# Kernel optimization log

Measured on AMD Instinct MI355X. Metric: run time of the kernel, lower is better.

## Reference

```python
import jax, jax.numpy as jnp
import numpy as np


def setup_inputs() -> dict:
    key = jax.random.key(0)
    ks = jax.random.split(key, 7)
    B, P, D = 4, 2048, 1024
    s = 1.0 / np.sqrt(D)
    return {
        "x":  jax.random.normal(ks[0], (B, P, D), dtype=jnp.float32),
        "Wq": jax.random.normal(ks[1], (D, D), dtype=jnp.float32) * s,
        "bq": jnp.zeros((D,), dtype=jnp.float32),
        "Wk": jax.random.normal(ks[2], (D, D), dtype=jnp.float32) * s,
        "bk": jnp.zeros((D,), dtype=jnp.float32),
        "Wv": jax.random.normal(ks[3], (D, D), dtype=jnp.float32) * s,
        "bv": jnp.zeros((D,), dtype=jnp.float32),
    }


def reference(x, Wq, bq, Wk, bk, Wv, bv):
    # x: [B, P, D]; Linear uses W stored torch-style [out, in]: y = x @ W.T + b
    b, p, d = x.shape
    q = jnp.einsum("bpd,ed->bpe", x, Wq) + bq
    k = jnp.einsum("bpd,ed->bpe", x, Wk) + bk
    v = jnp.einsum("bpd,ed->bpe", x, Wv) + bv
    attn = jnp.einsum("bqd,bkd->bqk", q, k)  # [B, P, P]
    causal = jnp.triu(jnp.ones((p, p), dtype=bool), k=1)  # True above diagonal
    attn = jnp.where(causal, -jnp.inf, attn)
    attn = attn / jnp.sqrt(jnp.asarray(d, dtype=attn.dtype))
    scores = jax.nn.softmax(attn, axis=-1)
    # dropout is identity in eval/deterministic mode
    return jnp.einsum("bqk,bkd->bqd", scores, v)
```

## Files before the change

kernel.cpp:

```cpp
#include <hip/hip_runtime.h>
#include <hip/hip_bf16.h>


typedef __attribute__((ext_vector_type(8))) short bf16x8;
typedef __attribute__((ext_vector_type(4))) float f32x4;

__device__ __forceinline__ unsigned short f2bf(float f) {
    union { float f; unsigned u; } v; v.f = f;
    unsigned r = v.u + 0x7FFF + ((v.u >> 16) & 1);
    return (unsigned short)(r >> 16);
}

__device__ __forceinline__ void gload_lds16(const unsigned short* g, unsigned short* l) {
    __builtin_amdgcn_global_load_lds(
        (const __attribute__((address_space(1))) unsigned int*)g,
        (__attribute__((address_space(3))) unsigned int*)l, 16, 0, 0);
}

__global__ void convert_kernel(const float* __restrict__ x,  const float* __restrict__ wq,
                               const float* __restrict__ wk, const float* __restrict__ wv,
                               const float* __restrict__ bq, const float* __restrict__ bk,
                               const float* __restrict__ bv,
                               unsigned short* __restrict__ xb, unsigned short* __restrict__ wqkvb,
                               float* __restrict__ bqkv, float* __restrict__ lsum) {
    long t = (long)blockIdx.x * blockDim.x + threadIdx.x;
    long idx = t * 4;
    const float* src; unsigned short* dst; long off;
    if      (idx <  8388608) { src = x;  dst = xb;            off = idx;            }
    else if (idx <  9437184) { src = wq; dst = wqkvb;         off = idx -  8388608; }
    else if (idx < 10485760) { src = wk; dst = wqkvb+1048576; off = idx -  9437184; }
    else if (idx < 11534336) { src = wv; dst = wqkvb+2097152; off = idx - 10485760; }
    else return;
    float4 v = *(const float4*)(src + off);
    ushort4 o = make_ushort4(f2bf(v.x), f2bf(v.y), f2bf(v.z), f2bf(v.w));
    *(ushort4*)(dst + off) = o;
    if (t < 768) {
        long o2 = t * 4;
        float4 b;
        if      (o2 < 1024) b = *(const float4*)(bq + o2);
        else if (o2 < 2048) b = *(const float4*)(bk + o2 - 1024);
        else                b = *(const float4*)(bv + o2 - 2048);
        *(float4*)(bqkv + o2) = b;
    }
    if (t >= 1024 && t < 3072) {
        float4 z = make_float4(0.f, 0.f, 0.f, 0.f);
        *(float4*)(lsum + (t - 1024) * 4) = z;
    }
}

__device__ __forceinline__ void stage(const unsigned short* gA, long lda,
                                      const unsigned short* gB, long ldb,
                                      unsigned short* As, unsigned short* Bs,
                                      int w, int k0) {
#pragma unroll
    for (int s = 0; s < 4; ++s) {
        gload_lds16(gA + k0 + (long)(s * 8) * lda, &As[(w * 32 + s * 8) * 64]);
        gload_lds16(gB + k0 + (long)(s * 8) * ldb, &Bs[(w * 32 + s * 8) * 64]);
    }
}

template<bool SWAP>
__device__ __forceinline__ void mfma_tile(const unsigned short* As, const unsigned short* Bs,
                                          int wr, int wc, int ln, int pr0, int pr1,
                                          f32x4 (&acc)[4][4]) {
#pragma unroll
    for (int kk = 0; kk < 2; ++kk) {
        const int pr = kk ? pr1 : pr0;
        bf16x8 af[4], bfr[4];
#pragma unroll
        for (int i = 0; i < 4; ++i)
            af[i] = *(const bf16x8*)(&As[(wr + i * 16 + ln) * 64 + pr]);
#pragma unroll
        for (int j = 0; j < 4; ++j)
            bfr[j] = *(const bf16x8*)(&Bs[(wc + j * 16 + ln) * 64 + pr]);
#pragma unroll
        for (int i = 0; i < 4; ++i)
#pragma unroll
            for (int j = 0; j < 4; ++j)
                acc[i][j] = SWAP
                    ? __builtin_amdgcn_mfma_f32_16x16x32_bf16(bfr[j], af[i], acc[i][j], 0, 0, 0)
                    : __builtin_amdgcn_mfma_f32_16x16x32_bf16(af[i], bfr[j], acc[i][j], 0, 0, 0);
    }
}

template<bool SWAP>
__device__ __forceinline__ void kloop_db(const unsigned short* gA, long lda,
                                         const unsigned short* gB, long ldb,
                                         unsigned short* As0, unsigned short* Bs0,
                                         unsigned short* As1, unsigned short* Bs1,
                                         int w, int lane, int Keff, f32x4 (&acc)[4][4]) {
    const int q  = lane >> 4;
    const int ln = lane & 15;
    const int wr = (w >> 1) * 64;
    const int wc = (w & 1) * 64;
    const int pr0 = ((q)     ^ (ln & 7)) * 8;
    const int pr1 = ((q + 4) ^ (ln & 7)) * 8;
    stage(gA, lda, gB, ldb, As0, Bs0, w, 0);
    __syncthreads();
    for (int k0 = 0; k0 < Keff; k0 += 128) {
        stage(gA, lda, gB, ldb, As1, Bs1, w, k0 + 64);
        mfma_tile<SWAP>(As0, Bs0, wr, wc, ln, pr0, pr1, acc);
        __syncthreads();
        if (k0 + 128 < Keff)
            stage(gA, lda, gB, ldb, As0, Bs0, w, k0 + 128);
        mfma_tile<SWAP>(As1, Bs1, wr, wc, ln, pr0, pr1, acc);
        __syncthreads();
    }
}

__global__ __launch_bounds__(256, 2)
void gemm_qkv(const unsigned short* __restrict__ X,
              const unsigned short* __restrict__ W,
              unsigned short* __restrict__ QK,
              unsigned short* __restrict__ VT,
              const float* __restrict__ bias) {
    const int n0 = blockIdx.x * 128;
    const int m0 = blockIdx.y * 128;
    __shared__ __align__(16) unsigned short As0[128 * 64], Bs0[128 * 64];
    __shared__ __align__(16) unsigned short As1[128 * 64], Bs1[128 * 64];
    const int tid = threadIdx.x, lane = tid & 63, w = tid >> 6;
    const int q = lane >> 4, ln = lane & 15;
    const int wr = (w >> 1) * 64, wc = (w & 1) * 64;
    const int srow = lane >> 3, sc = (lane & 7) ^ srow;
    const unsigned short* gA = X + (long)(m0 + w * 32 + srow) * 1024 + sc * 8;
    const unsigned short* gB = W + (long)(n0 + w * 32 + srow) * 1024 + sc * 8;
    f32x4 acc[4][4] = {};
    if (n0 >= 2048) {
        kloop_db<false>(gA, 1024, gB, 1024, As0, Bs0, As1, Bs1, w, lane, 1024, acc);
#pragma unroll
        for (int j = 0; j < 4; ++j) {
            const int e = n0 - 2048 + wc + j * 16 + ln;
            const float bc = bias[n0 + wc + j * 16 + ln];
#pragma unroll
            for (int i = 0; i < 4; ++i) {
                const int m = m0 + wr + i * 16 + q * 4;
                ushort4 o = make_ushort4(f2bf(acc[i][j][0] + bc), f2bf(acc[i][j][1] + bc),
                                         f2bf(acc[i][j][2] + bc), f2bf(acc[i][j][3] + bc));
                *(ushort4*)(VT + (long)e * 8192 + m) = o;
            }
        }
    } else {
        kloop_db<true>(gA, 1024, gB, 1024, As0, Bs0, As1, Bs1, w, lane, 1024, acc);
#pragma unroll
        for (int j = 0; j < 4; ++j) {
            const float4 bc = *(const float4*)(bias + n0 + wc + j * 16 + q * 4);
#pragma unroll
            for (int i = 0; i < 4; ++i) {
                const int m = m0 + wr + i * 16 + ln;
                const int n = n0 + wc + j * 16 + q * 4;
                ushort4 o = make_ushort4(f2bf(acc[i][j][0] + bc.x), f2bf(acc[i][j][1] + bc.y),
                                         f2bf(acc[i][j][2] + bc.z), f2bf(acc[i][j][3] + bc.w));
                *(ushort4*)(QK + (long)m * 2048 + n) = o;
            }
        }
    }
}

__global__ __launch_bounds__(256, 2)
void gemm_scores(const unsigned short* __restrict__ QK,
                 unsigned short* __restrict__ P,
                 float* __restrict__ lsum) {
    const int t = blockIdx.x;
    int i = (int)((sqrtf(8.0f * t + 1.0f) - 1.0f) * 0.5f);
    while ((i + 1) * (i + 2) / 2 <= t) ++i;
    while (i * (i + 1) / 2 > t) --i;
    const int j = t - i * (i + 1) / 2;
    const int m0 = i * 128, n0 = j * 128, z = blockIdx.y;
    const unsigned short* Qz = QK + (long)z * 2048 * 2048;
    const unsigned short* Kz = Qz + 1024;
    unsigned short* Pz = P + (long)z * 2048 * 2048;
    float* lz = lsum + z * 2048;

    __shared__ __align__(16) unsigned short As0[128 * 64], Bs0[128 * 64];
    __shared__ __align__(16) unsigned short As1[128 * 64], Bs1[128 * 64];
    const int tid = threadIdx.x, lane = tid & 63, w = tid >> 6;
    const int q = lane >> 4, ln = lane & 15;
    const int wr = (w >> 1) * 64, wc = (w & 1) * 64;
    const int srow = lane >> 3, sc = (lane & 7) ^ srow;
    const unsigned short* gA = Qz + (long)(m0 + w * 32 + srow) * 2048 + sc * 8;
    const unsigned short* gB = Kz + (long)(n0 + w * 32 + srow) * 2048 + sc * 8;
    f32x4 acc[4][4] = {};
    kloop_db<true>(gA, 2048, gB, 2048, As0, Bs0, As1, Bs1, w, lane, 1024, acc);

    const float scale = 0.03125f;
#pragma unroll
    for (int i2 = 0; i2 < 4; ++i2) {
        const int m = m0 + wr + i2 * 16 + ln;
        float rs = 0.f;
#pragma unroll
        for (int j2 = 0; j2 < 4; ++j2) {
            const int n = n0 + wc + j2 * 16 + q * 4;
            float p0 = (n     <= m) ? __expf(acc[i2][j2][0] * scale) : 0.f;
            float p1 = (n + 1 <= m) ? __expf(acc[i2][j2][1] * scale) : 0.f;
            float p2 = (n + 2 <= m) ? __expf(acc[i2][j2][2] * scale) : 0.f;
            float p3 = (n + 3 <= m) ? __expf(acc[i2][j2][3] * scale) : 0.f;
            rs += (p0 + p1) + (p2 + p3);
            ushort4 o = make_ushort4(f2bf(p0), f2bf(p1), f2bf(p2), f2bf(p3));
            *(ushort4*)(Pz + (long)m * 2048 + n) = o;
        }
        rs += __shfl_xor(rs, 16); rs += __shfl_xor(rs, 32);
        if (lane < 16) atomicAdd(&lz[m], rs);
    }
}

__global__ __launch_bounds__(256, 2)
void gemm_pv(const unsigned short* __restrict__ P,
             const unsigned short* __restrict__ VT,
             const float* __restrict__ lsum,
             float* __restrict__ out) {
    const int L  = blockIdx.x;
    const int ph = L >> 8;
    const int c  = L & 255;
    const int z  = c >> 6;
    const int r  = c & 63;
    const int mh = r >> 3;
    const int nt = r & 7;
    const int mt = ph ? 15 - mh : mh;
    const int m0 = mt * 128, n0 = nt * 128;
    const int Keff = m0 + 128;
    const unsigned short* Pz = P + (long)z * 2048 * 2048;
    const unsigned short* Vz = VT + (long)z * 2048;
    const float* lz = lsum + z * 2048;

    __shared__ __align__(16) unsigned short As0[128 * 64], Bs0[128 * 64];
    __shared__ __align__(16) unsigned short As1[128 * 64], Bs1[128 * 64];
    const int tid = threadIdx.x, lane = tid & 63, w = tid >> 6;
    const int q = lane >> 4, ln = lane & 15;
    const int wr = (w >> 1) * 64, wc = (w & 1) * 64;
    const int srow = lane >> 3, sc = (lane & 7) ^ srow;
    const unsigned short* gA = Pz + (long)(m0 + w * 32 + srow) * 2048 + sc * 8;
    const unsigned short* gB = Vz + (long)(n0 + w * 32 + srow) * 8192 + sc * 8;
    f32x4 acc[4][4] = {};
    kloop_db<true>(gA, 2048, gB, 8192, As0, Bs0, As1, Bs1, w, lane, Keff, acc);

#pragma unroll
    for (int i2 = 0; i2 < 4; ++i2) {
        const int m = m0 + wr + i2 * 16 + ln;
        const float inv = 1.0f / lz[m];
#pragma unroll
        for (int j2 = 0; j2 < 4; ++j2) {
            const int n = n0 + wc + j2 * 16 + q * 4;
            float4 o = make_float4(acc[i2][j2][0] * inv, acc[i2][j2][1] * inv,
                                   acc[i2][j2][2] * inv, acc[i2][j2][3] * inv);
            *(float4*)(out + (long)(z * 2048 + m) * 1024 + n) = o;
        }
    }
}

extern "C" void kernel_launch(void* const* d_in, const int* in_sizes, int n_in,
                              void* d_out, int out_size, void* d_ws, size_t ws_size,
                              hipStream_t stream) {
    const float* x  = (const float*)d_in[0];
    const float* Wq = (const float*)d_in[1];
    const float* bq = (const float*)d_in[2];
    const float* Wk = (const float*)d_in[3];
    const float* bk = (const float*)d_in[4];
    const float* Wv = (const float*)d_in[5];
    const float* bv = (const float*)d_in[6];
    float* out = (float*)d_out;

    char* ws = (char*)d_ws;
    unsigned short* xb    = (unsigned short*)ws; ws += (long)8192 * 1024 * 2;
    unsigned short* wqkvb = (unsigned short*)ws; ws += (long)3072 * 1024 * 2;
    float*          bqkv  = (float*)ws;          ws += (long)3072 * 4;
    float*          lsum  = (float*)ws;          ws += (long)8192 * 4;
    unsigned short* QKb   = (unsigned short*)ws; ws += (long)8192 * 2048 * 2;
    unsigned short* VTb   = (unsigned short*)ws; ws += (long)1024 * 8192 * 2;
    unsigned short* Pb    = (unsigned short*)ws; ws += (long)4 * 2048 * 2048 * 2;

    hipLaunchKernelGGL(convert_kernel, dim3(11264), dim3(256), 0, stream,
                       x, Wq, Wk, Wv, bq, bk, bv, xb, wqkvb, bqkv, lsum);

    hipLaunchKernelGGL(gemm_qkv, dim3(24, 64, 1), dim3(256), 0, stream,
                       xb, wqkvb, QKb, VTb, bqkv);

    hipLaunchKernelGGL(gemm_scores, dim3(136, 4, 1), dim3(256), 0, stream,
                       QKb, Pb, lsum);

    hipLaunchKernelGGL(gemm_pv, dim3(512, 1, 1), dim3(256), 0, stream,
                       Pb, VTb, lsum, out);
}
```

Measured before the change: 240.2 us.

## Replace QKV projection GEMM with 256x256-tile, 4-stage pipelined kernel

Rewrites the QKV projection GEMM to use 256x256 output tiles with 512 threads (8 waves), a 4-deep ring of LDS buffers (K-step 32) loaded via global_load_lds, and explicit vmcnt waits with s_setprio around the MFMA block. Larger tiles raise arithmetic intensity and cut global traffic. Deeper prefetch is meant to hide memory latency better than the previous double buffer. The cost is 128KB of dynamic LDS per block and only 384 blocks, so at most one block fits per CU and tail imbalance may grow.

Measured after the change: 256.9 us. 1.07x slower.

```diff
diff --git a/kernel.cpp b/kernel.cpp
--- a/kernel.cpp
+++ b/kernel.cpp
@@ -48,6 +48,107 @@
     }
 }
 
+__device__ __forceinline__ void stage256(const unsigned short* gA, const unsigned short* gB,
+                                         unsigned short* lds, int sdst, int t) {
+    unsigned short* dst = lds + (t & 3) * 16384;
+    const long koff = (long)t * 32;
+    gload_lds16(gA + koff,              dst + sdst);
+    gload_lds16(gA + koff + 128 * 1024, dst + 4096 + sdst);
+    gload_lds16(gB + koff,              dst + 8192 + sdst);
+    gload_lds16(gB + koff + 128 * 1024, dst + 12288 + sdst);
+}
+
+template<bool SWAP>
+__device__ __forceinline__ void qkv256_core(const unsigned short* gA, const unsigned short* gB,
+                                            unsigned short* lds, int sdst,
+                                            int arow, int brow, int fch,
+                                            f32x4 (&acc)[8][4]) {
+    stage256(gA, gB, lds, sdst, 0);
+    stage256(gA, gB, lds, sdst, 1);
+    stage256(gA, gB, lds, sdst, 2);
+    asm volatile("s_waitcnt vmcnt(8)" ::: "memory");
+    __builtin_amdgcn_s_barrier();
+#pragma unroll 1
+    for (int t = 0; t < 32; ++t) {
+        if (t + 3 < 32) stage256(gA, gB, lds, sdst, t + 3);
+        const unsigned short* Ab = lds + (t & 3) * 16384;
+        const unsigned short* Bb = Ab + 8192;
+        bf16x8 af[8], bf[4];
+#pragma unroll
+        for (int i = 0; i < 8; ++i)
+            af[i] = *(const bf16x8*)(Ab + (arow + i * 16) * 32 + fch);
+#pragma unroll
+        for (int j = 0; j < 4; ++j)
+            bf[j] = *(const bf16x8*)(Bb + (brow + j * 16) * 32 + fch);
+        __builtin_amdgcn_s_setprio(1);
+#pragma unroll
+        for (int i = 0; i < 8; ++i)
+#pragma unroll
+            for (int j = 0; j < 4; ++j)
+                acc[i][j] = SWAP
+                    ? __builtin_amdgcn_mfma_f32_16x16x32_bf16(bf[j], af[i], acc[i][j], 0, 0, 0)
+                    : __builtin_amdgcn_mfma_f32_16x16x32_bf16(af[i], bf[j], acc[i][j], 0, 0, 0);
+        __builtin_amdgcn_s_setprio(0);
+        if (t <= 28)      asm volatile("s_waitcnt vmcnt(8)" ::: "memory");
+        else if (t == 29) asm volatile("s_waitcnt vmcnt(4)" ::: "memory");
+        else if (t == 30) asm volatile("s_waitcnt vmcnt(0)" ::: "memory");
+        if (t < 31) __builtin_amdgcn_s_barrier();
+    }
+}
+
+__global__ __launch_bounds__(512, 2)
+void gemm_qkv256(const unsigned short* __restrict__ X,
+                 const unsigned short* __restrict__ W,
+                 unsigned short* __restrict__ QK,
+                 unsigned short* __restrict__ VT,
+                 const float* __restrict__ bias) {
+    extern __shared__ unsigned short lds[];
+    const int n0 = blockIdx.x * 256;
+    const int m0 = blockIdx.y * 256;
+    const int tid = threadIdx.x, lane = tid & 63, w = tid >> 6;
+    const int q = lane >> 4, ln = lane & 15;
+    const int wm = w >> 2, wn = w & 3;
+    const int srow = tid >> 2;
+    const int sch  = (((tid & 3) ^ (srow & 3)) << 3);
+    const unsigned short* gA = X + (long)(m0 + srow) * 1024 + sch;
+    const unsigned short* gB = W + (long)(n0 + srow) * 1024 + sch;
+    const int sdst = tid * 8;
+    const int arow = wm * 128 + ln;
+    const int brow = wn * 64 + ln;
+    const int fch  = ((q ^ (ln & 3)) << 3);
+    f32x4 acc[8][4] = {};
+    if (n0 >= 2048) {
+        qkv256_core<false>(gA, gB, lds, sdst, arow, brow, fch, acc);
+#pragma unroll
+        for (int j = 0; j < 4; ++j) {
+            const int ecol = n0 + wn * 64 + j * 16 + ln;
+            const float bc = bias[ecol];
+            const int e = ecol - 2048;
+#pragma unroll
+            for (int i = 0; i < 8; ++i) {
+                const int m = m0 + wm * 128 + i * 16 + q * 4;
+                ushort4 o = make_ushort4(f2bf(acc[i][j][0] + bc), f2bf(acc[i][j][1] + bc),
+                                         f2bf(acc[i][j][2] + bc), f2bf(acc[i][j][3] + bc));
+                *(ushort4*)(VT + (long)e * 8192 + m) = o;
+            }
+        }
+    } else {
+        qkv256_core<true>(gA, gB, lds, sdst, arow, brow, fch, acc);
+#pragma unroll
+        for (int j = 0; j < 4; ++j) {
+            const float4 bc = *(const float4*)(bias + n0 + wn * 64 + j * 16 + q * 4);
+#pragma unroll
+            for (int i = 0; i < 8; ++i) {
+                const int m = m0 + wm * 128 + i * 16 + ln;
+                const int n = n0 + wn * 64 + j * 16 + q * 4;
+                ushort4 o = make_ushort4(f2bf(acc[i][j][0] + bc.x), f2bf(acc[i][j][1] + bc.y),
+                                         f2bf(acc[i][j][2] + bc.z), f2bf(acc[i][j][3] + bc.w));
+                *(ushort4*)(QK + (long)m * 2048 + n) = o;
+            }
+        }
+    }
+}
+
 __device__ __forceinline__ void stage(const unsigned short* gA, long lda,
                                       const unsigned short* gB, long ldb,
                                       unsigned short* As, unsigned short* Bs,
@@ -109,54 +210,6 @@
 }
 
 __global__ __launch_bounds__(256, 2)
-void gemm_qkv(const unsigned short* __restrict__ X,
-              const unsigned short* __restrict__ W,
-              unsigned short* __restrict__ QK,
-              unsigned short* __restrict__ VT,
-              const float* __restrict__ bias) {
-    const int n0 = blockIdx.x * 128;
-    const int m0 = blockIdx.y * 128;
-    __shared__ __align__(16) unsigned short As0[128 * 64], Bs0[128 * 64];
-    __shared__ __align__(16) unsigned short As1[128 * 64], Bs1[128 * 64];
-    const int tid = threadIdx.x, lane = tid & 63, w = tid >> 6;
-    const int q = lane >> 4, ln = lane & 15;
-    const int wr = (w >> 1) * 64, wc = (w & 1) * 64;
-    const int srow = lane >> 3, sc = (lane & 7) ^ srow;
-    const unsigned short* gA = X + (long)(m0 + w * 32 + srow) * 1024 + sc * 8;
-    const unsigned short* gB = W + (long)(n0 + w * 32 + srow) * 1024 + sc * 8;
-    f32x4 acc[4][4] = {};
-    if (n0 >= 2048) {
-        kloop_db<false>(gA, 1024, gB, 1024, As0, Bs0, As1, Bs1, w, lane, 1024, acc);
-#pragma unroll
-        for (int j = 0; j < 4; ++j) {
-            const int e = n0 - 2048 + wc + j * 16 + ln;
-            const float bc = bias[n0 + wc + j * 16 + ln];
-#pragma unroll
-            for (int i = 0; i < 4; ++i) {
-                const int m = m0 + wr + i * 16 + q * 4;
-                ushort4 o = make_ushort4(f2bf(acc[i][j][0] + bc), f2bf(acc[i][j][1] + bc),
-                                         f2bf(acc[i][j][2] + bc), f2bf(acc[i][j][3] + bc));
-                *(ushort4*)(VT + (long)e * 8192 + m) = o;
-            }
-        }
-    } else {
-        kloop_db<true>(gA, 1024, gB, 1024, As0, Bs0, As1, Bs1, w, lane, 1024, acc);
-#pragma unroll
-        for (int j = 0; j < 4; ++j) {
-            const float4 bc = *(const float4*)(bias + n0 + wc + j * 16 + q * 4);
-#pragma unroll
-            for (int i = 0; i < 4; ++i) {
-                const int m = m0 + wr + i * 16 + ln;
-                const int n = n0 + wc + j * 16 + q * 4;
-                ushort4 o = make_ushort4(f2bf(acc[i][j][0] + bc.x), f2bf(acc[i][j][1] + bc.y),
-                                         f2bf(acc[i][j][2] + bc.z), f2bf(acc[i][j][3] + bc.w));
-                *(ushort4*)(QK + (long)m * 2048 + n) = o;
-            }
-        }
-    }
-}
-
-__global__ __launch_bounds__(256, 2)
 void gemm_scores(const unsigned short* __restrict__ QK,
                  unsigned short* __restrict__ P,
                  float* __restrict__ lsum) {
@@ -268,10 +321,13 @@
     unsigned short* VTb   = (unsigned short*)ws; ws += (long)1024 * 8192 * 2;
     unsigned short* Pb    = (unsigned short*)ws; ws += (long)4 * 2048 * 2048 * 2;
 
+    hipFuncSetAttribute((const void*)gemm_qkv256,
+                        hipFuncAttributeMaxDynamicSharedMemorySize, 131072);
+
     hipLaunchKernelGGL(convert_kernel, dim3(11264), dim3(256), 0, stream,
                        x, Wq, Wk, Wv, bq, bk, bv, xb, wqkvb, bqkv, lsum);
 
-    hipLaunchKernelGGL(gemm_qkv, dim3(24, 64, 1), dim3(256), 0, stream,
+    hipLaunchKernelGGL(gemm_qkv256, dim3(12, 32, 1), dim3(512), 131072, stream,
                        xb, wqkvb, QKb, VTb, bqkv);
 
     hipLaunchKernelGGL(gemm_scores, dim3(136, 4, 1), dim3(256), 0, stream,
```
